# Optimization experiments

Measured on AMD Instinct MI355X. Metric: run time of the kernel, lower is better.

## Reference

```python
import jax, jax.numpy as jnp
import numpy as np

POOLED_H = 7
POOLED_W = 7
SPATIAL_SCALE = 0.0625
B, C, H, W = 8, 256, 48, 48
R = 300
IMG = 768  # = H / SPATIAL_SCALE


def setup_inputs() -> dict:
    key = jax.random.key(0)
    k1, k2, k3, k4 = jax.random.split(key, 4)
    features = jax.random.normal(k1, (B, C, H, W), dtype=jnp.float32)
    # rois: (batch_idx, x1, y1, x2, y2) in input-image coords
    bidx = jax.random.randint(k2, (R, 1), 0, B).astype(jnp.float32)
    tl = jax.random.uniform(k3, (R, 2), minval=0.0, maxval=IMG - 64.0)
    wh = jax.random.uniform(k4, (R, 2), minval=32.0, maxval=320.0)
    br = jnp.minimum(tl + wh, IMG - 1.0)
    rois = jnp.concatenate([bidx, tl, br], axis=1).astype(jnp.float32)
    return {"features": features, "rois": rois}


def _hat_integral(x, grid):
    """Integral from -inf to x of the unit hat basis function centered at each
    grid point g (support [g-1, g+1], peak 1, total mass 1).
    x: [..., 1-broadcastable], grid: [G] -> returns [..., G]."""
    t = x[..., None] - (grid - 1.0)
    return jnp.where(
        t <= 0.0, 0.0,
        jnp.where(t <= 1.0, 0.5 * t * t,
                  jnp.where(t <= 2.0, 1.0 - 0.5 * (2.0 - t) ** 2, 1.0)))


def reference(features, rois):
    # Precise RoI Pooling: exact double integral of the bilinear interpolant
    # over each bin, divided by bin area. Bilinear interp (with zero padding
    # outside the map, as in the CUDA PrRoIPoolingGetData) is
    #   f(u,v) = sum_{j,i} feat[j,i] * hat_j(v) * hat_i(u)
    # so the bin integral factorizes into per-axis hat-integral weights.
    Bf, Cf, Hf, Wf = features.shape
    bidx = rois[:, 0].astype(jnp.int32)
    x1 = rois[:, 1] * SPATIAL_SCALE
    y1 = rois[:, 2] * SPATIAL_SCALE
    x2 = rois[:, 3] * SPATIAL_SCALE
    y2 = rois[:, 4] * SPATIAL_SCALE
    roi_w = jnp.maximum(x2 - x1, 0.0)
    roi_h = jnp.maximum(y2 - y1, 0.0)
    bin_w = roi_w / POOLED_W  # [R]
    bin_h = roi_h / POOLED_H

    ph = jnp.arange(POOLED_H, dtype=jnp.float32)
    pw = jnp.arange(POOLED_W, dtype=jnp.float32)
    ya = y1[:, None] + ph[None, :] * bin_h[:, None]  # [R, PH]
    yb = ya + bin_h[:, None]
    xa = x1[:, None] + pw[None, :] * bin_w[:, None]  # [R, PW]
    xb = xa + bin_w[:, None]

    gy = jnp.arange(Hf, dtype=jnp.float32)
    gx = jnp.arange(Wf, dtype=jnp.float32)
    Wy = _hat_integral(yb, gy) - _hat_integral(ya, gy)  # [R, PH, H]
    Wx = _hat_integral(xb, gx) - _hat_integral(xa, gx)  # [R, PW, W]

    feat = features[bidx]  # [R, C, H, W]
    t = jnp.einsum('rpj,rcji->rcpi', Wy, feat)   # integrate over y
    num = jnp.einsum('rqi,rcpi->rcpq', Wx, t)    # integrate over x -> [R,C,PH,PW]

    area = (bin_w * bin_h)[:, None, None, None]  # win_size per ROI
    out = jnp.where(area > 0.0, num / jnp.where(area > 0.0, area, 1.0), 0.0)
    return out
```

## Files before the change

### kernel.cpp

```cpp
#include <hip/hip_runtime.h>


#define PH 7
#define PW 7
#define NBINS 49
#define SCALE 0.0625f
#define CH 256
#define FH 48
#define FW 48
#define RNUM 300
#define CB 8
#define MAXJ 23
#define ROWF 28

__device__ __forceinline__ float hat_int(float x, float g) {
    float t = x - (g - 1.0f);
    if (t <= 0.0f) return 0.0f;
    if (t <= 1.0f) return 0.5f * t * t;
    if (t <= 2.0f) { float u = 2.0f - t; return 1.0f - 0.5f * u * u; }
    return 1.0f;
}

__global__ __launch_bounds__(256)
void prroi_fused(const float* __restrict__ feat,
                 const float* __restrict__ rois,
                 float* __restrict__ out) {
    const int cblk = blockIdx.x;
    const int r    = blockIdx.y;
    const int c0   = cblk * CB;
    const int tid  = threadIdx.x;

    __shared__ float patch[MAXJ * ROWF * CB];
    __shared__ float rs[PW * MAXJ * CB];
    __shared__ float pbuf[99];

    const float* roi = rois + r * 5;
    const float f0 = roi[0], f1 = roi[1], f2 = roi[2], f3 = roi[3], f4 = roi[4];
    const int   b  = (int)f0;
    const float x1 = f1 * SCALE, y1 = f2 * SCALE;
    const float x2 = f3 * SCALE, y2 = f4 * SCALE;
    const float ylo = fminf(y1, y2), yhi = fmaxf(y1, y2);
    const float xlo = fminf(x1, x2), xhi = fmaxf(x1, x2);
    const int j1 = min(FH - 1, (int)floorf(yhi) + 1);
    const int i1 = min(FW - 1, (int)floorf(xhi) + 1);
    const int J0 = min(max(0, (int)floorf(ylo) - 1), FH - 6);
    const int I0 = min(max(0, (int)floorf(xlo) - 1) & ~3, FW - 8);
    const int JROWS = min(FH - J0, max(j1 - J0 + 1, 6));
    int NI4 = min(((i1 - I0) >> 2) + 1, (FW - I0) >> 2);
    NI4 = max(NI4, 2);

    const float* fb = feat + (size_t)(b * CH + c0) * FH * FW;
    const int J7 = JROWS * 7;
    for (int u = tid; u < 2 * J7; u += 256) {
        const int q  = (u >= J7) ? 1 : 0;
        const int rm = u - q * J7;
        const int j  = rm / 7;
        const int i4 = rm - j * 7;
        if (i4 < NI4) {
            const int ig = I0 + 4 * i4;
            const float* src = fb + ((size_t)(4 * q) * FH + (J0 + j)) * FW + ig;
            const float4 v0  = *(const float4*)(src);
            const float4 v1v = *(const float4*)(src + FH * FW);
            const float4 v2v = *(const float4*)(src + 2 * FH * FW);
            const float4 v3v = *(const float4*)(src + 3 * FH * FW);
            float* dst = &patch[((size_t)j * ROWF + 4 * i4) * CB + 4 * q];
            *(float4*)(dst + 0 * CB) = make_float4(v0.x, v1v.x, v2v.x, v3v.x);
            *(float4*)(dst + 1 * CB) = make_float4(v0.y, v1v.y, v2v.y, v3v.y);
            *(float4*)(dst + 2 * CB) = make_float4(v0.z, v1v.z, v2v.z, v3v.z);
            *(float4*)(dst + 3 * CB) = make_float4(v0.w, v1v.w, v2v.w, v3v.w);
        }
    }

    if (tid < PH) {
        const float roi_h = fmaxf(y2 - y1, 0.0f);
        const float bin_h = roi_h / (float)PH;
        const int ph = tid;
        const float ya = y1 + ph * bin_h, yb = ya + bin_h;
        const int base = min(max((int)floorf(ya) - 1, J0), J0 + JROWS - 6);
        pbuf[84 + ph] = __int_as_float(base - J0);
#pragma unroll
        for (int k = 0; k < 6; ++k) {
            const float g = (float)(base + k);
            pbuf[ph * 6 + k] = hat_int(yb, g) - hat_int(ya, g);
        }
    } else if (tid < PH + PW) {
        const float roi_w = fmaxf(x2 - x1, 0.0f);
        const float bin_w = roi_w / (float)PW;
        const int pw = tid - PH;
        const float xa = x1 + pw * bin_w, xb = xa + bin_w;
        const int base = min(max((int)floorf(xa) - 1, I0), I0 + 4 * NI4 - 6);
        pbuf[91 + pw] = __int_as_float(base - I0);
#pragma unroll
        for (int k = 0; k < 6; ++k) {
            const float g = (float)(base + k);
            pbuf[42 + pw * 6 + k] = hat_int(xb, g) - hat_int(xa, g);
        }
    } else if (tid == PH + PW) {
        const float roi_w = fmaxf(x2 - x1, 0.0f);
        const float roi_h = fmaxf(y2 - y1, 0.0f);
        const float area = (roi_w / (float)PW) * (roi_h / (float)PH);
        pbuf[98] = (area > 0.0f) ? (1.0f / area) : 0.0f;
    }
    __syncthreads();

    const int nA = JROWS * 14;
    {
        const int v1 = tid;
        if (v1 < nA) {
            const int j = v1 / 14; const int rem = v1 - j * 14;
            const int pw = rem >> 1, q = rem & 1;
            const int bi = __float_as_int(pbuf[91 + pw]);
            const float* base = &patch[((size_t)j * ROWF + bi) * CB + 4 * q];
            float ax = 0.0f, ay = 0.0f, az = 0.0f, aw = 0.0f;
#pragma unroll
            for (int ii = 0; ii < 6; ++ii) {
                const float w = pbuf[42 + pw * 6 + ii];
                const float4 v = *(const float4*)(base + ii * CB);
                ax += w * v.x; ay += w * v.y; az += w * v.z; aw += w * v.w;
            }
            *(float4*)(&rs[((size_t)pw * MAXJ + j) * CB + 4 * q]) =
                make_float4(ax, ay, az, aw);
        }
        const int v2 = tid + 256;
        if (v2 < nA) {
            const int j = v2 / 14; const int rem = v2 - j * 14;
            const int pw = rem >> 1, q = rem & 1;
            const int bi = __float_as_int(pbuf[91 + pw]);
            const float* base = &patch[((size_t)j * ROWF + bi) * CB + 4 * q];
            float ax = 0.0f, ay = 0.0f, az = 0.0f, aw = 0.0f;
#pragma unroll
            for (int ii = 0; ii < 6; ++ii) {
                const float w = pbuf[42 + pw * 6 + ii];
                const float4 v = *(const float4*)(base + ii * CB);
                ax += w * v.x; ay += w * v.y; az += w * v.z; aw += w * v.w;
            }
            *(float4*)(&rs[((size_t)pw * MAXJ + j) * CB + 4 * q]) =
                make_float4(ax, ay, az, aw);
        }
    }
    __syncthreads();

    const int bin = tid & 63;
    const int cp  = tid >> 6;
    if (bin < NBINS) {
        const int phv = bin / PW, pwv = bin - phv * PW;
        const int bj = __float_as_int(pbuf[84 + phv]);
        const float inv_area = pbuf[98];
        const float* rbase = &rs[((size_t)pwv * MAXJ + bj) * CB + 2 * cp];
        float ax = 0.0f, ay = 0.0f;
#pragma unroll
        for (int jj = 0; jj < 6; ++jj) {
            const float w = pbuf[phv * 6 + jj];
            const float2 v = *(const float2*)(rbase + jj * CB);
            ax += w * v.x; ay += w * v.y;
        }
        float* o = out + ((size_t)r * CH + c0 + 2 * cp) * NBINS + bin;
        o[0]     = ax * inv_area;
        o[NBINS] = ay * inv_area;
    }
}

extern "C" void kernel_launch(void* const* d_in, const int* in_sizes, int n_in,
                              void* d_out, int out_size, void* d_ws, size_t ws_size,
                              hipStream_t stream) {
    const float* feat = (const float*)d_in[0];
    const float* rois = (const float*)d_in[1];
    float* out = (float*)d_out;
    (void)d_ws; (void)ws_size;

    prroi_fused<<<dim3(CH / CB, RNUM), 256, 0, stream>>>(feat, rois, out);
}
```

Before: 92.31 us.

## Swizzle shared-memory patch layout and compute x-weights in registers per thread

Reorganizes the shared feature patch into 32-float lines per (row, 4-column group) with an XOR swizzle on the float4 slot. The row-sum buffer gets a parity-based swizzle as well, to reduce LDS bank conflicts in the x-integration and y-integration stages. The per-bin x hat-integral weights and base offsets are now computed directly in each thread's registers before the load loop, instead of by 7 threads into shared memory. This removes those shared reads but duplicates the hat-weight arithmetic across threads and adds index math to every LDS access.

```diff
diff --git a/kernel.cpp b/kernel.cpp
--- a/kernel.cpp
+++ b/kernel.cpp
@@ -11,7 +11,7 @@
 #define RNUM 300
 #define CB 8
 #define MAXJ 23
-#define ROWF 28
+#define NL 7
 
 __device__ __forceinline__ float hat_int(float x, float g) {
     float t = x - (g - 1.0f);
@@ -30,15 +30,14 @@
     const int c0   = cblk * CB;
     const int tid  = threadIdx.x;
 
-    __shared__ float patch[MAXJ * ROWF * CB];
+    __shared__ float patch[MAXJ * NL * 32];
     __shared__ float rs[PW * MAXJ * CB];
     __shared__ float pbuf[99];
 
     const float* roi = rois + r * 5;
-    const float f0 = roi[0], f1 = roi[1], f2 = roi[2], f3 = roi[3], f4 = roi[4];
-    const int   b  = (int)f0;
-    const float x1 = f1 * SCALE, y1 = f2 * SCALE;
-    const float x2 = f3 * SCALE, y2 = f4 * SCALE;
+    const int   b  = (int)roi[0];
+    const float x1 = roi[1] * SCALE, y1 = roi[2] * SCALE;
+    const float x2 = roi[3] * SCALE, y2 = roi[4] * SCALE;
     const float ylo = fminf(y1, y2), yhi = fmaxf(y1, y2);
     const float xlo = fminf(x1, x2), xhi = fmaxf(x1, x2);
     const int j1 = min(FH - 1, (int)floorf(yhi) + 1);
@@ -49,13 +48,43 @@
     int NI4 = min(((i1 - I0) >> 2) + 1, (FW - I0) >> 2);
     NI4 = max(NI4, 2);
 
+    const float roi_w = fmaxf(x2 - x1, 0.0f);
+    const float bin_w = roi_w / (float)PW;
+    const int nA = JROWS * 14;
+    int pw1 = 0, q1 = 0, j1r = 0, pw2 = 0, q2 = 0, j2r = 0, bi1 = 0, bi2 = 0;
+    float wxa[6], wxb[6];
+    const bool a1 = tid < nA, a2 = (tid + 256) < nA;
+    if (a1) {
+        j1r = tid / 14; const int rem = tid - j1r * 14; pw1 = rem >> 1; q1 = rem & 1;
+        const float xa = x1 + pw1 * bin_w, xb = xa + bin_w;
+        const int base = min(max((int)floorf(xa) - 1, I0), I0 + 4 * NI4 - 6);
+        bi1 = base - I0;
+#pragma unroll
+        for (int k = 0; k < 6; ++k) {
+            const float g = (float)(base + k);
+            wxa[k] = hat_int(xb, g) - hat_int(xa, g);
+        }
+    }
+    if (a2) {
+        const int v2 = tid + 256;
+        j2r = v2 / 14; const int rem = v2 - j2r * 14; pw2 = rem >> 1; q2 = rem & 1;
+        const float xa = x1 + pw2 * bin_w, xb = xa + bin_w;
+        const int base = min(max((int)floorf(xa) - 1, I0), I0 + 4 * NI4 - 6);
+        bi2 = base - I0;
+#pragma unroll
+        for (int k = 0; k < 6; ++k) {
+            const float g = (float)(base + k);
+            wxb[k] = hat_int(xb, g) - hat_int(xa, g);
+        }
+    }
+
     const float* fb = feat + (size_t)(b * CH + c0) * FH * FW;
-    const int J7 = JROWS * 7;
+    const int J7 = JROWS * NL;
     for (int u = tid; u < 2 * J7; u += 256) {
         const int q  = (u >= J7) ? 1 : 0;
         const int rm = u - q * J7;
-        const int j  = rm / 7;
-        const int i4 = rm - j * 7;
+        const int j  = rm / NL;
+        const int i4 = rm - j * NL;
         if (i4 < NI4) {
             const int ig = I0 + 4 * i4;
             const float* src = fb + ((size_t)(4 * q) * FH + (J0 + j)) * FW + ig;
@@ -63,17 +92,18 @@
             const float4 v1v = *(const float4*)(src + FH * FW);
             const float4 v2v = *(const float4*)(src + 2 * FH * FW);
             const float4 v3v = *(const float4*)(src + 3 * FH * FW);
-            float* dst = &patch[((size_t)j * ROWF + 4 * i4) * CB + 4 * q];
-            *(float4*)(dst + 0 * CB) = make_float4(v0.x, v1v.x, v2v.x, v3v.x);
-            *(float4*)(dst + 1 * CB) = make_float4(v0.y, v1v.y, v2v.y, v3v.y);
-            *(float4*)(dst + 2 * CB) = make_float4(v0.z, v1v.z, v2v.z, v3v.z);
-            *(float4*)(dst + 3 * CB) = make_float4(v0.w, v1v.w, v2v.w, v3v.w);
+            const int msk = (j + i4) & 7;
+            float* dl = &patch[(j * NL + i4) * 32];
+            *(float4*)(dl + (((0 | q) ^ msk) << 2)) = make_float4(v0.x, v1v.x, v2v.x, v3v.x);
+            *(float4*)(dl + (((2 | q) ^ msk) << 2)) = make_float4(v0.y, v1v.y, v2v.y, v3v.y);
+            *(float4*)(dl + (((4 | q) ^ msk) << 2)) = make_float4(v0.z, v1v.z, v2v.z, v3v.z);
+            *(float4*)(dl + (((6 | q) ^ msk) << 2)) = make_float4(v0.w, v1v.w, v2v.w, v3v.w);
         }
     }
 
+    const float roi_h = fmaxf(y2 - y1, 0.0f);
+    const float bin_h = roi_h / (float)PH;
     if (tid < PH) {
-        const float roi_h = fmaxf(y2 - y1, 0.0f);
-        const float bin_h = roi_h / (float)PH;
         const int ph = tid;
         const float ya = y1 + ph * bin_h, yb = ya + bin_h;
         const int base = min(max((int)floorf(ya) - 1, J0), J0 + JROWS - 6);
@@ -83,60 +113,39 @@
             const float g = (float)(base + k);
             pbuf[ph * 6 + k] = hat_int(yb, g) - hat_int(ya, g);
         }
-    } else if (tid < PH + PW) {
-        const float roi_w = fmaxf(x2 - x1, 0.0f);
-        const float bin_w = roi_w / (float)PW;
-        const int pw = tid - PH;
-        const float xa = x1 + pw * bin_w, xb = xa + bin_w;
-        const int base = min(max((int)floorf(xa) - 1, I0), I0 + 4 * NI4 - 6);
-        pbuf[91 + pw] = __int_as_float(base - I0);
-#pragma unroll
-        for (int k = 0; k < 6; ++k) {
-            const float g = (float)(base + k);
-            pbuf[42 + pw * 6 + k] = hat_int(xb, g) - hat_int(xa, g);
-        }
-    } else if (tid == PH + PW) {
-        const float roi_w = fmaxf(x2 - x1, 0.0f);
-        const float roi_h = fmaxf(y2 - y1, 0.0f);
-        const float area = (roi_w / (float)PW) * (roi_h / (float)PH);
+    } else if (tid == PH) {
+        const float area = bin_w * bin_h;
         pbuf[98] = (area > 0.0f) ? (1.0f / area) : 0.0f;
     }
     __syncthreads();
 
-    const int nA = JROWS * 14;
-    {
-        const int v1 = tid;
-        if (v1 < nA) {
-            const int j = v1 / 14; const int rem = v1 - j * 14;
-            const int pw = rem >> 1, q = rem & 1;
-            const int bi = __float_as_int(pbuf[91 + pw]);
-            const float* base = &patch[((size_t)j * ROWF + bi) * CB + 4 * q];
-            float ax = 0.0f, ay = 0.0f, az = 0.0f, aw = 0.0f;
+    if (a1) {
+        float ax = 0.0f, ay = 0.0f, az = 0.0f, aw = 0.0f;
 #pragma unroll
-            for (int ii = 0; ii < 6; ++ii) {
-                const float w = pbuf[42 + pw * 6 + ii];
-                const float4 v = *(const float4*)(base + ii * CB);
-                ax += w * v.x; ay += w * v.y; az += w * v.z; aw += w * v.w;
-            }
-            *(float4*)(&rs[((size_t)pw * MAXJ + j) * CB + 4 * q]) =
-                make_float4(ax, ay, az, aw);
+        for (int ii = 0; ii < 6; ++ii) {
+            const float w = wxa[ii];
+            const int i  = bi1 + ii;
+            const int i4 = i >> 2, il = i & 3;
+            const int slot = ((il << 1) | q1) ^ ((j1r + i4) & 7);
+            const float4 v = *(const float4*)(&patch[(j1r * NL + i4) * 32 + (slot << 2)]);
+            ax += w * v.x; ay += w * v.y; az += w * v.z; aw += w * v.w;
         }
-        const int v2 = tid + 256;
-        if (v2 < nA) {
-            const int j = v2 / 14; const int rem = v2 - j * 14;
-            const int pw = rem >> 1, q = rem & 1;
-            const int bi = __float_as_int(pbuf[91 + pw]);
-            const float* base = &patch[((size_t)j * ROWF + bi) * CB + 4 * q];
-            float ax = 0.0f, ay = 0.0f, az = 0.0f, aw = 0.0f;
+        *(float4*)(&rs[((size_t)pw1 * MAXJ + j1r) * CB + ((q1 ^ (j1r & 1)) << 2)]) =
+            make_float4(ax, ay, az, aw);
+    }
+    if (a2) {
+        float ax = 0.0f, ay = 0.0f, az = 0.0f, aw = 0.0f;
 #pragma unroll
-            for (int ii = 0; ii < 6; ++ii) {
-                const float w = pbuf[42 + pw * 6 + ii];
-                const float4 v = *(const float4*)(base + ii * CB);
-                ax += w * v.x; ay += w * v.y; az += w * v.z; aw += w * v.w;
-            }
-            *(float4*)(&rs[((size_t)pw * MAXJ + j) * CB + 4 * q]) =
-                make_float4(ax, ay, az, aw);
+        for (int ii = 0; ii < 6; ++ii) {
+            const float w = wxb[ii];
+            const int i  = bi2 + ii;
+            const int i4 = i >> 2, il = i & 3;
+            const int slot = ((il << 1) | q2) ^ ((j2r + i4) & 7);
+            const float4 v = *(const float4*)(&patch[(j2r * NL + i4) * 32 + (slot << 2)]);
+            ax += w * v.x; ay += w * v.y; az += w * v.z; aw += w * v.w;
         }
+        *(float4*)(&rs[((size_t)pw2 * MAXJ + j2r) * CB + ((q2 ^ (j2r & 1)) << 2)]) =
+            make_float4(ax, ay, az, aw);
     }
     __syncthreads();
 
@@ -146,12 +155,14 @@
         const int phv = bin / PW, pwv = bin - phv * PW;
         const int bj = __float_as_int(pbuf[84 + phv]);
         const float inv_area = pbuf[98];
-        const float* rbase = &rs[((size_t)pwv * MAXJ + bj) * CB + 2 * cp];
+        const int qh = cp >> 1, lo = (cp & 1) * 2;
         float ax = 0.0f, ay = 0.0f;
 #pragma unroll
         for (int jj = 0; jj < 6; ++jj) {
+            const int j = bj + jj;
             const float w = pbuf[phv * 6 + jj];
-            const float2 v = *(const float2*)(rbase + jj * CB);
+            const float2 v = *(const float2*)(
+                &rs[((size_t)pwv * MAXJ + j) * CB + ((qh ^ (j & 1)) << 2) + lo]);
             ax += w * v.x; ay += w * v.y;
         }
         float* o = out + ((size_t)r * CH + c0 + 2 * cp) * NBINS + bin;
```

Measured after the change: 93.19 us. No clear change (+1.0%).
